# Performance work log

Hardware: AMD Instinct MI355X
Metric: run time of the kernel (lower is better)

The kernel has to match this reference:

```python
import jax, jax.numpy as jnp
import numpy as np


def _orthogonal_matrix(vectors):
    # Q = I @ H1 @ H2 @ ... ; each H = I - 2 v v^T applied as a rank-1 update:
    # Q @ H = Q - 2 (Q v) v^T  (same math as explicit matmul, O(d^2) per reflection)
    dim = vectors.shape[1]
    eye = jnp.eye(dim, dtype=vectors.dtype)

    def step(Q, v):
        vn = v / (jnp.linalg.norm(v) + 1e-8)
        Q = Q - 2.0 * jnp.outer(Q @ vn, vn)
        return Q, None

    Q, _ = jax.lax.scan(step, eye, vectors)
    return Q


def setup_inputs() -> dict:
    key = jax.random.key(0)
    k1, k2 = jax.random.split(key)
    dim, n_reflections, batch = 2048, 30, 16384
    x = jax.random.normal(k1, (batch, dim), dtype=jnp.float32)
    vectors = jax.random.normal(k2, (n_reflections, dim), dtype=jnp.float32)
    bias = jnp.zeros((dim,), dtype=jnp.float32)
    return {"x": x, "vectors": vectors, "bias": bias}


def reference(x, vectors, bias):
    Q = _orthogonal_matrix(vectors)      # [dim, dim]
    return x @ Q + bias                  # [batch, dim]
```

## Files before the change

kernel.cpp:

```cpp
#include <hip/hip_runtime.h>
#include <math.h>

#define DIM   2048
#define NREF  30
#define KPAD  32
#define BATCH 16384

typedef __attribute__((ext_vector_type(8))) short short8;
typedef __attribute__((ext_vector_type(4))) float f32x4;
typedef __attribute__((ext_vector_type(2))) float f32x2;

#define WS_VN   0
#define WS_G    61440
#define WS_T    62464
#define WS_FP1  63488
#define WS_S    96256

__device__ __forceinline__ unsigned short f2bf(float f) {
    unsigned u = __float_as_uint(f);
    u += 0x7FFF + ((u >> 16) & 1);
    return (unsigned short)(u >> 16);
}

__global__ void k_prep(const float* __restrict__ vec, float* __restrict__ vn,
                       float* __restrict__ G) {
    int b = blockIdx.x, t = threadIdx.x;
    __shared__ float wsum[3][4];
    if (b < NREF) {
        const float* v = vec + b * DIM;
        float s = 0.f;
        for (int d = t; d < DIM; d += 256) { float xv = v[d]; s += xv * xv; }
        #pragma unroll
        for (int off = 32; off > 0; off >>= 1) s += __shfl_down(s, off);
        if ((t & 63) == 0) wsum[0][t >> 6] = s;
        __syncthreads();
        float tot = wsum[0][0] + wsum[0][1] + wsum[0][2] + wsum[0][3];
        float scale = 1.f / (sqrtf(tot) + 1e-8f);
        float* o = vn + b * DIM;
        for (int d = t; d < DIM; d += 256) o[d] = v[d] * scale;
    } else {
        int idx = b - NREF;
        int i = idx / NREF, j = idx % NREF;
        const float* a = vec + i * DIM;
        const float* c = vec + j * DIM;
        float sab = 0.f, saa = 0.f, sbb = 0.f;
        for (int d = t; d < DIM; d += 256) {
            float av = a[d], cv = c[d];
            sab += av * cv; saa += av * av; sbb += cv * cv;
        }
        #pragma unroll
        for (int off = 32; off > 0; off >>= 1) {
            sab += __shfl_down(sab, off);
            saa += __shfl_down(saa, off);
            sbb += __shfl_down(sbb, off);
        }
        if ((t & 63) == 0) { wsum[0][t >> 6] = sab; wsum[1][t >> 6] = saa; wsum[2][t >> 6] = sbb; }
        __syncthreads();
        if (t == 0) {
            float tab = wsum[0][0] + wsum[0][1] + wsum[0][2] + wsum[0][3];
            float taa = wsum[1][0] + wsum[1][1] + wsum[1][2] + wsum[1][3];
            float tbb = wsum[2][0] + wsum[2][1] + wsum[2][2] + wsum[2][3];
            G[i * NREF + j] = tab / ((sqrtf(taa) + 1e-8f) * (sqrtf(tbb) + 1e-8f));
        }
    }
}

__global__ void k_T2(const float* __restrict__ G, float* __restrict__ T) {
    int t = threadIdx.x;
    __shared__ float Gs[NREF * NREF];
    __shared__ float Ts[NREF][NREF];
    for (int idx = t; idx < NREF * NREF; idx += 64) {
        Gs[idx] = G[idx];
        Ts[idx / NREF][idx % NREF] = 0.f;
    }
    __syncthreads();
    if (t < NREF) {
        Ts[t][t] = 2.f;
        for (int j = t + 1; j < NREF; j++) {
            float val = 0.f;
            for (int mm = t; mm < j; mm++) val += Ts[t][mm] * Gs[mm * NREF + j];
            Ts[t][j] = -2.f * val;
        }
    }
    __syncthreads();
    for (int idx = t; idx < NREF * NREF; idx += 64) T[idx] = Ts[idx / NREF][idx % NREF];
}

__global__ void k_mid(const float* __restrict__ vn, const float* __restrict__ T,
                      unsigned short* __restrict__ fp1) {
    int b = blockIdx.x, t = threadIdx.x;
    __shared__ float W2s[256][33];
    int d = b * 256 + t;
    float vr[NREF];
    #pragma unroll
    for (int j = 0; j < NREF; j++) vr[j] = vn[j * DIM + d];
    #pragma unroll
    for (int k = 0; k < KPAD; k++) {
        float acc = 0.f;
        if (k < NREF)
            for (int j = 0; j <= k; j++) acc += vr[j] * T[j * NREF + k];
        W2s[t][k] = acc;
    }
    __syncthreads();
    short8* out = (short8*)fp1;
    #pragma unroll
    for (int u = 0; u < 4; u++) {
        int lf = t * 4 + u;
        int ks_l = lf >> 7, nt = (lf >> 6) & 1, lane = lf & 63;
        int q = lane >> 4, n = lane & 15;
        short8 v;
        #pragma unroll
        for (int j = 0; j < 8; j++)
            v[j] = (short)f2bf(W2s[ks_l * 32 + q * 8 + j][nt * 16 + n]);
        out[((b * 8 + ks_l) * 2 + nt) * 64 + lane] = v;
    }
}

__global__ __launch_bounds__(256) void k_p1(const float* __restrict__ x,
                                            const short8* __restrict__ fp1,
                                            float* __restrict__ S) {
    int tid = threadIdx.x;
    int wave = tid >> 6, lane = tid & 63;
    int m = lane & 15, q = lane >> 4;
    int r0 = blockIdx.x * 16;
    int kb = wave * 512;

    const float* xp = x + (size_t)(r0 + m) * DIM + kb + q * 8;

    f32x4 acc0 = {0.f, 0.f, 0.f, 0.f};
    f32x4 acc1 = {0.f, 0.f, 0.f, 0.f};
    #pragma unroll 4
    for (int ks = 0; ks < 16; ks++) {
        f32x4 xa = *(const f32x4*)(xp + ks * 32);
        f32x4 xb = *(const f32x4*)(xp + ks * 32 + 4);
        short8 a;
        a[0] = (short)f2bf(xa[0]); a[1] = (short)f2bf(xa[1]);
        a[2] = (short)f2bf(xa[2]); a[3] = (short)f2bf(xa[3]);
        a[4] = (short)f2bf(xb[0]); a[5] = (short)f2bf(xb[1]);
        a[6] = (short)f2bf(xb[2]); a[7] = (short)f2bf(xb[3]);
        int ksg = wave * 16 + ks;
        short8 b0 = fp1[(ksg * 2 + 0) * 64 + lane];
        short8 b1 = fp1[(ksg * 2 + 1) * 64 + lane];
        acc0 = __builtin_amdgcn_mfma_f32_16x16x32_bf16(a, b0, acc0, 0, 0, 0);
        acc1 = __builtin_amdgcn_mfma_f32_16x16x32_bf16(a, b1, acc1, 0, 0, 0);
    }

    __shared__ f32x4 red[4][64][2];
    red[wave][lane][0] = acc0;
    red[wave][lane][1] = acc1;
    __syncthreads();
    if (tid < 64) {
        f32x4 s0 = red[0][tid][0], s1 = red[0][tid][1];
        #pragma unroll
        for (int w = 1; w < 4; w++) { s0 += red[w][tid][0]; s1 += red[w][tid][1]; }
        int mq = tid & 15, qq = tid >> 4;
        #pragma unroll
        for (int reg = 0; reg < 4; reg++) {
            size_t row = r0 + qq * 4 + reg;
            S[row * KPAD + mq]      = s0[reg];
            S[row * KPAD + 16 + mq] = s1[reg];
        }
    }
}

__global__ __launch_bounds__(256) void k_p2(const float* __restrict__ x,
                                            const float* __restrict__ S,
                                            const float* __restrict__ vn,
                                            const float* __restrict__ bias,
                                            float* __restrict__ y) {
    __shared__ float Stile[32 * KPAD];
    int tid = threadIdx.x;
    int wave = tid >> 6, lane = tid & 63;
    int rc = blockIdx.x >> 2;
    int cg = blockIdx.x & 3;
    int r0 = rc * 32;
    int cl = cg * 512 + wave * 128 + lane * 2;

    ((f32x4*)Stile)[tid] = ((const f32x4*)(S + (size_t)r0 * KPAD))[tid];

    f32x2 vt[NREF];
    #pragma unroll
    for (int n = 0; n < NREF; n++)
        vt[n] = *(const f32x2*)(vn + n * DIM + cl);
    f32x2 bi = *(const f32x2*)(bias + cl);
    __syncthreads();

    const float* xp = x + (size_t)r0 * DIM + cl;
    float* yp = y + (size_t)r0 * DIM + cl;
    #pragma unroll 4
    for (int r = 0; r < 32; r++) {
        f32x2 xv = *(const f32x2*)(xp + (size_t)r * DIM);
        f32x2 acc = xv + bi;
        const float* Sr = &Stile[r * KPAD];
        #pragma unroll
        for (int n = 0; n < NREF; n++) {
            float sn = Sr[n];
            acc -= sn * vt[n];
        }
        *(f32x2*)(yp + (size_t)r * DIM) = acc;
    }
}

extern "C" void kernel_launch(void* const* d_in, const int* in_sizes, int n_in,
                              void* d_out, int out_size, void* d_ws, size_t ws_size,
                              hipStream_t stream) {
    const float* x    = (const float*)d_in[0];
    const float* vec  = (const float*)d_in[1];
    const float* bias = (const float*)d_in[2];
    float* out = (float*)d_out;
    float* ws  = (float*)d_ws;

    float* vn = ws + WS_VN;
    float* G  = ws + WS_G;
    float* T  = ws + WS_T;
    unsigned short* fp1 = (unsigned short*)(ws + WS_FP1);
    float* S = ws + WS_S;

    k_prep<<<NREF + NREF * NREF, 256, 0, stream>>>(vec, vn, G);
    k_T2<<<1, 64, 0, stream>>>(G, T);
    k_mid<<<8, 256, 0, stream>>>(vn, T, fp1);
    k_p1<<<BATCH / 16, 256, 0, stream>>>(x, (const short8*)fp1, S);
    k_p2<<<2048, 256, 0, stream>>>(x, S, vn, bias, out);
}
```

Baseline: 290.8 us.

## Stage x tiles into LDS with async global_load_lds double buffering in k_p1

Rewrites the projection kernel k_p1 to copy each 16-row tile of x into LDS in 256-column chunks using direct global-to-LDS loads, double-buffered so the next chunk and its weight fragments load while the current one is used by MFMA. Each wave's global reads now cover contiguous full rows instead of strided 32-byte pieces, with the K dimension split across waves inside each chunk. The aim is better coalescing and hiding of load latency in this memory-bound pass over x. In exchange it adds about 33KB of LDS per block, which may lower occupancy, plus two barriers per chunk and hand-written vmcnt waits that depend on an exact count of outstanding loads.

```diff
diff --git a/kernel.cpp b/kernel.cpp
--- a/kernel.cpp
+++ b/kernel.cpp
@@ -9,6 +9,9 @@
 typedef __attribute__((ext_vector_type(8))) short short8;
 typedef __attribute__((ext_vector_type(4))) float f32x4;
 typedef __attribute__((ext_vector_type(2))) float f32x2;
+
+typedef const __attribute__((address_space(1))) void* gas1_t;
+typedef __attribute__((address_space(3))) void* las3_t;
 
 #define WS_VN   0
 #define WS_G    61440
@@ -119,33 +122,83 @@
 __global__ __launch_bounds__(256) void k_p1(const float* __restrict__ x,
                                             const short8* __restrict__ fp1,
                                             float* __restrict__ S) {
+    __shared__ float xs[2][16][260];
+    __shared__ f32x4 red[4][64][2];
     int tid = threadIdx.x;
     int wave = tid >> 6, lane = tid & 63;
     int m = lane & 15, q = lane >> 4;
     int r0 = blockIdx.x * 16;
-    int kb = wave * 512;
-
-    const float* xp = x + (size_t)(r0 + m) * DIM + kb + q * 8;
+
+    const char* xbase = (const char*)(x + (size_t)r0 * DIM);
+
+    auto STAGE = [&](int c, int b) {
+        #pragma unroll
+        for (int i = 0; i < 4; i++) {
+            int r = wave * 4 + i;
+            const char* g = xbase + (size_t)r * (DIM * 4) + c * 1024 + (size_t)(lane * 16);
+            __builtin_amdgcn_global_load_lds((gas1_t)g, (las3_t)((char*)&xs[b][r][0]),
+                                             16, 0, 0);
+        }
+    };
+
+    short8 f0a, f0b, f1a, f1b, n0a, n0b, n1a, n1b;
+    {
+        int ksg = wave * 2;
+        f0a = fp1[(ksg * 2 + 0) * 64 + lane];
+        f0b = fp1[(ksg * 2 + 1) * 64 + lane];
+        f1a = fp1[((ksg + 1) * 2 + 0) * 64 + lane];
+        f1b = fp1[((ksg + 1) * 2 + 1) * 64 + lane];
+    }
+    STAGE(0, 0);
 
     f32x4 acc0 = {0.f, 0.f, 0.f, 0.f};
     f32x4 acc1 = {0.f, 0.f, 0.f, 0.f};
-    #pragma unroll 4
-    for (int ks = 0; ks < 16; ks++) {
-        f32x4 xa = *(const f32x4*)(xp + ks * 32);
-        f32x4 xb = *(const f32x4*)(xp + ks * 32 + 4);
-        short8 a;
-        a[0] = (short)f2bf(xa[0]); a[1] = (short)f2bf(xa[1]);
-        a[2] = (short)f2bf(xa[2]); a[3] = (short)f2bf(xa[3]);
-        a[4] = (short)f2bf(xb[0]); a[5] = (short)f2bf(xb[1]);
-        a[6] = (short)f2bf(xb[2]); a[7] = (short)f2bf(xb[3]);
-        int ksg = wave * 16 + ks;
-        short8 b0 = fp1[(ksg * 2 + 0) * 64 + lane];
-        short8 b1 = fp1[(ksg * 2 + 1) * 64 + lane];
-        acc0 = __builtin_amdgcn_mfma_f32_16x16x32_bf16(a, b0, acc0, 0, 0, 0);
-        acc1 = __builtin_amdgcn_mfma_f32_16x16x32_bf16(a, b1, acc1, 0, 0, 0);
-    }
-
-    __shared__ f32x4 red[4][64][2];
+
+    #pragma unroll
+    for (int c = 0; c < 8; c++) {
+        int b = c & 1;
+        if (c < 7) {
+            int ksg = (c + 1) * 8 + wave * 2;
+            n0a = fp1[(ksg * 2 + 0) * 64 + lane];
+            n0b = fp1[(ksg * 2 + 1) * 64 + lane];
+            n1a = fp1[((ksg + 1) * 2 + 0) * 64 + lane];
+            n1b = fp1[((ksg + 1) * 2 + 1) * 64 + lane];
+            STAGE(c + 1, b ^ 1);
+            asm volatile("s_waitcnt vmcnt(8)" ::: "memory");
+        } else {
+            asm volatile("s_waitcnt vmcnt(0)" ::: "memory");
+        }
+        __builtin_amdgcn_s_barrier();
+        __builtin_amdgcn_sched_barrier(0);
+
+        const char* rb = (const char*)xs + b * 16640 + m * 1040 + q * 32;
+        {
+            f32x4 xa = *(const f32x4*)(rb + (wave * 2 + 0) * 128);
+            f32x4 xb = *(const f32x4*)(rb + (wave * 2 + 0) * 128 + 16);
+            short8 a;
+            a[0] = (short)f2bf(xa[0]); a[1] = (short)f2bf(xa[1]);
+            a[2] = (short)f2bf(xa[2]); a[3] = (short)f2bf(xa[3]);
+            a[4] = (short)f2bf(xb[0]); a[5] = (short)f2bf(xb[1]);
+            a[6] = (short)f2bf(xb[2]); a[7] = (short)f2bf(xb[3]);
+            acc0 = __builtin_amdgcn_mfma_f32_16x16x32_bf16(a, f0a, acc0, 0, 0, 0);
+            acc1 = __builtin_amdgcn_mfma_f32_16x16x32_bf16(a, f0b, acc1, 0, 0, 0);
+        }
+        {
+            f32x4 xa = *(const f32x4*)(rb + (wave * 2 + 1) * 128);
+            f32x4 xb = *(const f32x4*)(rb + (wave * 2 + 1) * 128 + 16);
+            short8 a;
+            a[0] = (short)f2bf(xa[0]); a[1] = (short)f2bf(xa[1]);
+            a[2] = (short)f2bf(xa[2]); a[3] = (short)f2bf(xa[3]);
+            a[4] = (short)f2bf(xb[0]); a[5] = (short)f2bf(xb[1]);
+            a[6] = (short)f2bf(xb[2]); a[7] = (short)f2bf(xb[3]);
+            acc0 = __builtin_amdgcn_mfma_f32_16x16x32_bf16(a, f1a, acc0, 0, 0, 0);
+            acc1 = __builtin_amdgcn_mfma_f32_16x16x32_bf16(a, f1b, acc1, 0, 0, 0);
+        }
+        __builtin_amdgcn_sched_barrier(0);
+        __builtin_amdgcn_s_barrier();
+        f0a = n0a; f0b = n0b; f1a = n1a; f1b = n1b;
+    }
+
     red[wave][lane][0] = acc0;
     red[wave][lane][1] = acc1;
     __syncthreads();
```

New measurement: 297.3 us. +2.2%, slower.

## Fuse projection and rank-update kernels so x rows are reused from cache

Applied to the files above, without the earlier changes.

Merges the two batch kernels (x·W projection via MFMA, then y = x + bias − S·Vn) into one kernel per 16-row block. The S coefficients stay in shared memory instead of round-tripping through global memory, and the second read of x should hit L2 because the same block just read those rows. Output stores become nontemporal. The trade-off is that each block now loops over 4 column passes and reloads the Vn slices per pass, with less parallelism per block in the update phase.

```diff
diff --git a/kernel.cpp b/kernel.cpp
--- a/kernel.cpp
+++ b/kernel.cpp
@@ -14,7 +14,6 @@
 #define WS_G    61440
 #define WS_T    62464
 #define WS_FP1  63488
-#define WS_S    96256
 
 __device__ __forceinline__ unsigned short f2bf(float f) {
     unsigned u = __float_as_uint(f);
@@ -116,88 +115,86 @@
     }
 }
 
-__global__ __launch_bounds__(256) void k_p1(const float* __restrict__ x,
-                                            const short8* __restrict__ fp1,
-                                            float* __restrict__ S) {
+__global__ __launch_bounds__(256, 4) void k_fused(const float* __restrict__ x,
+                                                  const short8* __restrict__ fp1,
+                                                  const float* __restrict__ vn,
+                                                  const float* __restrict__ bias,
+                                                  float* __restrict__ y) {
+    __shared__ f32x4 red[4][64][2];
+    __shared__ float Sf[16][KPAD];
     int tid = threadIdx.x;
     int wave = tid >> 6, lane = tid & 63;
     int m = lane & 15, q = lane >> 4;
     int r0 = blockIdx.x * 16;
-    int kb = wave * 512;
-
-    const float* xp = x + (size_t)(r0 + m) * DIM + kb + q * 8;
-
-    f32x4 acc0 = {0.f, 0.f, 0.f, 0.f};
-    f32x4 acc1 = {0.f, 0.f, 0.f, 0.f};
-    #pragma unroll 4
-    for (int ks = 0; ks < 16; ks++) {
-        f32x4 xa = *(const f32x4*)(xp + ks * 32);
-        f32x4 xb = *(const f32x4*)(xp + ks * 32 + 4);
-        short8 a;
-        a[0] = (short)f2bf(xa[0]); a[1] = (short)f2bf(xa[1]);
-        a[2] = (short)f2bf(xa[2]); a[3] = (short)f2bf(xa[3]);
-        a[4] = (short)f2bf(xb[0]); a[5] = (short)f2bf(xb[1]);
-        a[6] = (short)f2bf(xb[2]); a[7] = (short)f2bf(xb[3]);
-        int ksg = wave * 16 + ks;
-        short8 b0 = fp1[(ksg * 2 + 0) * 64 + lane];
-        short8 b1 = fp1[(ksg * 2 + 1) * 64 + lane];
-        acc0 = __builtin_amdgcn_mfma_f32_16x16x32_bf16(a, b0, acc0, 0, 0, 0);
-        acc1 = __builtin_amdgcn_mfma_f32_16x16x32_bf16(a, b1, acc1, 0, 0, 0);
-    }
-
-    __shared__ f32x4 red[4][64][2];
-    red[wave][lane][0] = acc0;
-    red[wave][lane][1] = acc1;
-    __syncthreads();
-    if (tid < 64) {
-        f32x4 s0 = red[0][tid][0], s1 = red[0][tid][1];
-        #pragma unroll
-        for (int w = 1; w < 4; w++) { s0 += red[w][tid][0]; s1 += red[w][tid][1]; }
-        int mq = tid & 15, qq = tid >> 4;
-        #pragma unroll
-        for (int reg = 0; reg < 4; reg++) {
-            size_t row = r0 + qq * 4 + reg;
-            S[row * KPAD + mq]      = s0[reg];
-            S[row * KPAD + 16 + mq] = s1[reg];
-        }
-    }
-}
-
-__global__ __launch_bounds__(256) void k_p2(const float* __restrict__ x,
-                                            const float* __restrict__ S,
-                                            const float* __restrict__ vn,
-                                            const float* __restrict__ bias,
-                                            float* __restrict__ y) {
-    __shared__ float Stile[32 * KPAD];
-    int tid = threadIdx.x;
-    int wave = tid >> 6, lane = tid & 63;
-    int rc = blockIdx.x >> 2;
-    int cg = blockIdx.x & 3;
-    int r0 = rc * 32;
-    int cl = cg * 512 + wave * 128 + lane * 2;
-
-    ((f32x4*)Stile)[tid] = ((const f32x4*)(S + (size_t)r0 * KPAD))[tid];
-
-    f32x2 vt[NREF];
-    #pragma unroll
-    for (int n = 0; n < NREF; n++)
-        vt[n] = *(const f32x2*)(vn + n * DIM + cl);
-    f32x2 bi = *(const f32x2*)(bias + cl);
-    __syncthreads();
-
-    const float* xp = x + (size_t)r0 * DIM + cl;
-    float* yp = y + (size_t)r0 * DIM + cl;
-    #pragma unroll 4
-    for (int r = 0; r < 32; r++) {
-        f32x2 xv = *(const f32x2*)(xp + (size_t)r * DIM);
-        f32x2 acc = xv + bi;
-        const float* Sr = &Stile[r * KPAD];
-        #pragma unroll
-        for (int n = 0; n < NREF; n++) {
-            float sn = Sr[n];
-            acc -= sn * vt[n];
-        }
-        *(f32x2*)(yp + (size_t)r * DIM) = acc;
+
+    {
+        int kb = wave * 512;
+        const float* xp = x + (size_t)(r0 + m) * DIM + kb + q * 8;
+
+        f32x4 acc0 = {0.f, 0.f, 0.f, 0.f};
+        f32x4 acc1 = {0.f, 0.f, 0.f, 0.f};
+        #pragma unroll 4
+        for (int ks = 0; ks < 16; ks++) {
+            f32x4 xa = *(const f32x4*)(xp + ks * 32);
+            f32x4 xb = *(const f32x4*)(xp + ks * 32 + 4);
+            short8 a;
+            a[0] = (short)f2bf(xa[0]); a[1] = (short)f2bf(xa[1]);
+            a[2] = (short)f2bf(xa[2]); a[3] = (short)f2bf(xa[3]);
+            a[4] = (short)f2bf(xb[0]); a[5] = (short)f2bf(xb[1]);
+            a[6] = (short)f2bf(xb[2]); a[7] = (short)f2bf(xb[3]);
+            int ksg = wave * 16 + ks;
+            short8 b0 = fp1[(ksg * 2 + 0) * 64 + lane];
+            short8 b1 = fp1[(ksg * 2 + 1) * 64 + lane];
+            acc0 = __builtin_amdgcn_mfma_f32_16x16x32_bf16(a, b0, acc0, 0, 0, 0);
+            acc1 = __builtin_amdgcn_mfma_f32_16x16x32_bf16(a, b1, acc1, 0, 0, 0);
+        }
+
+        red[wave][lane][0] = acc0;
+        red[wave][lane][1] = acc1;
+        __syncthreads();
+        if (tid < 64) {
+            f32x4 s0 = red[0][tid][0], s1 = red[0][tid][1];
+            #pragma unroll
+            for (int w = 1; w < 4; w++) { s0 += red[w][tid][0]; s1 += red[w][tid][1]; }
+            int mq = tid & 15, qq = tid >> 4;
+            #pragma unroll
+            for (int reg = 0; reg < 4; reg++) {
+                Sf[qq * 4 + reg][mq]      = s0[reg];
+                Sf[qq * 4 + reg][16 + mq] = s1[reg];
+            }
+        }
+        __syncthreads();
+    }
+
+    const float* xr = x + (size_t)r0 * DIM;
+    float* yr = y + (size_t)r0 * DIM;
+
+    #pragma unroll 1
+    for (int pass = 0; pass < 4; pass++) {
+        int cl = pass * 512 + tid * 2;
+        f32x2 vt[32];
+        #pragma unroll
+        for (int n = 0; n < NREF; n++)
+            vt[n] = *(const f32x2*)(vn + n * DIM + cl);
+        vt[30] = (f32x2){0.f, 0.f};
+        vt[31] = (f32x2){0.f, 0.f};
+        f32x2 bi = *(const f32x2*)(bias + cl);
+
+        #pragma unroll 4
+        for (int r = 0; r < 16; r++) {
+            f32x2 xv = *(const f32x2*)(xr + (size_t)r * DIM + cl);
+            f32x2 acc = xv + bi;
+            const float* Sr = &Sf[r][0];
+            #pragma unroll
+            for (int n4 = 0; n4 < 8; n4++) {
+                f32x4 s4 = *(const f32x4*)&Sr[n4 * 4];
+                acc -= s4[0] * vt[n4 * 4 + 0];
+                acc -= s4[1] * vt[n4 * 4 + 1];
+                acc -= s4[2] * vt[n4 * 4 + 2];
+                acc -= s4[3] * vt[n4 * 4 + 3];
+            }
+            __builtin_nontemporal_store(acc, (f32x2*)(yr + (size_t)r * DIM + cl));
+        }
     }
 }
 
@@ -214,11 +211,9 @@
     float* G  = ws + WS_G;
     float* T  = ws + WS_T;
     unsigned short* fp1 = (unsigned short*)(ws + WS_FP1);
-    float* S = ws + WS_S;
 
     k_prep<<<NREF + NREF * NREF, 256, 0, stream>>>(vec, vn, G);
     k_T2<<<1, 64, 0, stream>>>(G, T);
     k_mid<<<8, 256, 0, stream>>>(vn, T, fp1);
-    k_p1<<<BATCH / 16, 256, 0, stream>>>(x, (const short8*)fp1, S);
-    k_p2<<<2048, 256, 0, stream>>>(x, S, vn, bias, out);
-}
+    k_fused<<<BATCH / 16, 256, 0, stream>>>(x, (const short8*)fp1, vn, bias, out);
+}
```

Result: no change. 288.4 us (-0.8%).
